# Optimization experiments

Hardware: AMD Instinct MI355X
Metric: run time of the kernel (lower is better)

The kernel has to match this reference:

```python
import jax, jax.numpy as jnp
import numpy as np

B, S, D = 2, 2048, 512
H = 8            # num_attention_heads
CHUNK = 64       # chunk_size
WIN = 128        # retrospective_window / sliding window
NS = 5           # muon_ns_steps
FF = 2048        # intermediate_size
EPS = 1e-6       # RMSNorm eps


def _rms(x, w):
    return x * w * jax.lax.rsqrt(jnp.mean(x * x, axis=-1, keepdims=True) + EPS)


def _dwconv(x, w, b):
    # depthwise conv1d, kernel 3, pad 1. x: [b,s,d], w: [d,3], b: [d]
    xp = jnp.pad(x, ((0, 0), (1, 1), (0, 0)))
    return xp[:, :-2] * w[:, 0] + xp[:, 1:-1] * w[:, 1] + xp[:, 2:] * w[:, 2] + b


def _ns5(G):
    # Muon Newton-Schulz quintic orthogonalization on [b,d,d]
    a, b, c = 3.4445, -4.7750, 2.0315
    X = G / (jnp.linalg.norm(G, axis=(-2, -1), keepdims=True) + 1e-7)
    for _ in range(NS):
        A = X @ jnp.swapaxes(X, -2, -1)
        Bm = b * A + c * (A @ A)
        X = a * X + Bm @ X
    return X


def _swa(x, wq, wk, wv, wo):
    b, s, d = x.shape
    hd = d // H
    q = (x @ wq.T).reshape(b, s, H, hd)
    k = (x @ wk.T).reshape(b, s, H, hd)
    v = (x @ wv.T).reshape(b, s, H, hd)
    scores = jnp.einsum('bqhe,bkhe->bhqk', q, k) / np.float32(np.sqrt(hd))
    i = jnp.arange(s)[:, None]
    j = jnp.arange(s)[None, :]
    mask = (j <= i) & (i - j < WIN)
    scores = jnp.where(mask, scores, -jnp.inf)
    p = jax.nn.softmax(scores, axis=-1)
    o = jnp.einsum('bhqk,bkhe->bqhe', p, v).reshape(b, s, d)
    return o @ wo.T


def setup_inputs() -> dict:
    key = jax.random.key(0)
    ks = jax.random.split(key, 32)
    p = lambda i, shape, s=0.02: jax.random.normal(ks[i], shape, jnp.float32) * s
    inp = {
        'x': jax.random.normal(ks[0], (B, S, D), jnp.float32),
        'mem_state': jnp.zeros((B, D, D), jnp.float32),
        'buf_k': jnp.zeros((B, WIN, D), jnp.float32),
        'buf_v': jnp.zeros((B, WIN, D), jnp.float32),
        'nw_in': jnp.ones((D,), jnp.float32),
        'nw_kq': jnp.ones((D,), jnp.float32),
        'nw_out': jnp.ones((D,), jnp.float32),
        'wk_a': p(1, (D, D)), 'wq_a': p(2, (D, D)), 'wv_a': p(3, (D, D)),
        'wg': p(4, (3 * D, D)), 'wb': p(5, (D, D)),
        'ck_w': p(6, (D, 3), 0.3), 'ck_b': p(7, (D,), 0.02),
        'cq_w': p(8, (D, 3), 0.3), 'cq_b': p(9, (D,), 0.02),
        's1_wq': p(10, (D, D)), 's1_wk': p(11, (D, D)), 's1_wv': p(12, (D, D)), 's1_wo': p(13, (D, D)),
        's2_wq': p(14, (D, D)), 's2_wk': p(15, (D, D)), 's2_wv': p(16, (D, D)), 's2_wo': p(17, (D, D)),
        'n1_w': jnp.ones((D,), jnp.float32), 'n2_w': jnp.ones((D,), jnp.float32),
        'm_w1': p(18, (FF, D)), 'm_w2': p(19, (FF, D)), 'm_w3': p(20, (D, FF)),
    }
    return inp


def _atlas(x, mem_state, buf_k, buf_v, nw_in, nw_kq, nw_out,
           wk_a, wq_a, wv_a, wg, wb, ck_w, ck_b, cq_w, cq_b):
    b, s, d = x.shape
    xn = _rms(x, nw_in)
    v = jax.nn.silu(xn @ wv_a.T)
    k = _rms(jax.nn.silu(_dwconv(xn @ wk_a.T, ck_w, ck_b)), nw_kq)
    q = _rms(jax.nn.silu(_dwconv(xn @ wq_a.T, cq_w, cq_b)), nw_kq)
    gates = jax.nn.silu(xn @ wg.T)
    gamma, eta, alpha = jnp.split(gates, 3, axis=-1)
    bypass = jax.nn.silu(xn @ wb.T)

    n = s // CHUNK
    ch = lambda t: t.reshape(b, n, CHUNK, d).swapaxes(0, 1)  # [n,b,chunk,d]

    def body(carry, inp):
        M, bk, bv = carry
        ck_, cq_, cv_, ce_, ca_ = inp
        ctx_k = jnp.concatenate([bk, ck_], axis=1)
        ctx_v = jnp.concatenate([bv, cv_], axis=1)
        err = ctx_k @ M - ctx_v
        grad = jnp.einsum('bld,ble->bde', ctx_k, err)
        og = _ns5(grad)
        M = M * ca_.mean(axis=1, keepdims=True) - og * ce_.mean(axis=1, keepdims=True)
        return (M, ctx_k[:, -WIN:], ctx_v[:, -WIN:]), cq_ @ M

    (Mf, bkf, bvf), outs = jax.lax.scan(body, (mem_state, buf_k, buf_v),
                                        (ch(k), ch(q), ch(v), ch(eta), ch(alpha)))
    out = outs.swapaxes(0, 1).reshape(b, s, d)
    out = _rms(out, nw_out) * bypass * gamma
    return out, Mf, bkf, bvf


def reference(x, mem_state, buf_k, buf_v, nw_in, nw_kq, nw_out, wk_a, wq_a, wv_a,
              wg, wb, ck_w, ck_b, cq_w, cq_b, s1_wq, s1_wk, s1_wv, s1_wo,
              s2_wq, s2_wk, s2_wv, s2_wo, n1_w, n2_w, m_w1, m_w2, m_w3):
    mem_out, Mf, bkf, bvf = _atlas(x, mem_state, buf_k, buf_v, nw_in, nw_kq, nw_out,
                                   wk_a, wq_a, wv_a, wg, wb, ck_w, ck_b, cq_w, cq_b)
    mem_out = _rms(mem_out, n1_w)
    attn_out = _rms(_swa(x, s1_wq, s1_wk, s1_wv, s1_wo), n2_w)
    fused = mem_out + attn_out
    y = _swa(fused, s2_wq, s2_wk, s2_wv, s2_wo)
    mlp = (jax.nn.silu(y @ m_w1.T) * (y @ m_w2.T)) @ m_w3.T
    out = fused + mlp
    return (out, Mf, bkf, bvf)
```

## Files before the change

### kernel.cpp

```cpp
#include <hip/hip_runtime.h>
#include <hip/hip_bf16.h>

typedef __hip_bfloat16 bf16;
typedef __attribute__((ext_vector_type(8))) short bfrag;
typedef __attribute__((ext_vector_type(8))) unsigned short u16x8;
typedef __attribute__((ext_vector_type(4))) float f32x4;

#define SB 2
#define SS 2048
#define SD 512
#define SH 8
#define SWIN 128
#define SCH 64
#define SNCH 32
#define SFF 2048
#define KPROWS 2176
#define KPBATCH 1114112L
#define BSD 1048576L
#define DD 262144L
#define ERRN 98304L

__device__ __forceinline__ void stf(float* p, float v){ *p = v; }
__device__ __forceinline__ void stf(bf16* p, float v){ *p = __float2bfloat16(v); }

__device__ __forceinline__ unsigned short f2bs(float f){
  union { float f; unsigned int u; } v; v.f = f;
  unsigned int r = v.u + 0x7FFFu + ((v.u >> 16) & 1u);
  return (unsigned short)(r >> 16);
}
__device__ __forceinline__ float bs2f(unsigned short h){
  union { unsigned int u; float f; } v; v.u = ((unsigned int)h) << 16;
  return v.f;
}

__device__ __forceinline__ float block_sum256(float v, float* sbuf){
  #pragma unroll
  for (int o = 32; o > 0; o >>= 1) v += __shfl_xor(v, o);
  int wid = threadIdx.x >> 6;
  if ((threadIdx.x & 63) == 0) sbuf[wid] = v;
  __syncthreads();
  float r = sbuf[0] + sbuf[1] + sbuf[2] + sbuf[3];
  __syncthreads();
  return r;
}

enum { EPI_NONE=0, EPI_SILU=1, EPI_SUB=2, EPI_LINCOMB=3, EPI_MUL=4, EPI_ADD=5, EPI_SILU_MUL=6 };

template<bool TRA, bool TRB, int EPI, bool EPAIR, bool OSPLIT, bool OF32, bool FROB, bool MUPD, int SCL>
__global__ __launch_bounds__(256)
void sgemm32_k(const unsigned short* __restrict__ Ahl, const unsigned short* __restrict__ Bhl,
               float* __restrict__ Cf, unsigned short* __restrict__ Chl,
               const float* __restrict__ Ef, const unsigned short* __restrict__ Ehl,
               float* __restrict__ frobOut,
               const float* __restrict__ partIn, int nPart,
               float a0, float a1, int M, int N, int K,
               long sA, long pA, long sB, long pB,
               long sCf, long sChl, long pC, long sE, long pE,
               int lda, int ldb, int ldc, int lde,
               const float* __restrict__ alphaM, const float* __restrict__ etaM, int chunkIdx)
{
  __shared__ __align__(16) unsigned short As[2][2][32][40];
  __shared__ __align__(16) unsigned short Bs[2][2][32][40];
  __shared__ float fb[4];
  const int bz = blockIdx.z;
  const unsigned short* A = Ahl + (long)bz*sA;
  const unsigned short* B = Bhl + (long)bz*sB;
  const int bm = blockIdx.x*32, bn = blockIdx.y*32;
  const int tid = threadIdx.x;
  const int lane = tid & 63, wid = tid >> 6;
  const int wr = (wid >> 1)*16, wc = (wid & 1)*16;
  const int fm = lane & 15, fk = (lane >> 4)*8;

  int aR=0, aC=0, aPl=0, tK=0, tM0=0, tPl=0;
  if (!TRA) { aR = tid >> 3; int s = tid & 7; aPl = s >> 2; aC = (s & 3) << 3; }
  else      { tK = tid & 31; int q = tid >> 5; tPl = q >> 2; tM0 = (q & 3) << 3; }
  int bR=0, bC=0, bPl=0, uK=0, uN0=0, uPl=0;
  if (TRB)  { bR = tid >> 3; int s = tid & 7; bPl = s >> 2; bC = (s & 3) << 3; }
  else      { uK = tid & 31; int q = tid >> 5; uPl = q >> 2; uN0 = (q & 3) << 3; }

  u16x8 ra, rb;
  auto LA = [&](int k0){
    if (!TRA) ra = *reinterpret_cast<const u16x8*>(A + (long)(bm+aR)*lda + k0 + aC + (aPl ? pA : 0));
    else      ra = *reinterpret_cast<const u16x8*>(A + (long)(k0+tK)*lda + bm + tM0 + (tPl ? pA : 0));
  };
  auto SA = [&](int buf){
    if (!TRA) *reinterpret_cast<u16x8*>(&As[buf][aPl][aR][aC]) = ra;
    else {
      #pragma unroll
      for (int j=0;j<8;j++) As[buf][tPl][tM0+j][tK] = ra[j];
    }
  };
  auto LB = [&](int k0){
    if (TRB)  rb = *reinterpret_cast<const u16x8*>(B + (long)(bn+bR)*ldb + k0 + bC + (bPl ? pB : 0));
    else      rb = *reinterpret_cast<const u16x8*>(B + (long)(k0+uK)*ldb + bn + uN0 + (uPl ? pB : 0));
  };
  auto SBst = [&](int buf){
    if (TRB)  *reinterpret_cast<u16x8*>(&Bs[buf][bPl][bR][bC]) = rb;
    else {
      #pragma unroll
      for (int j=0;j<8;j++) Bs[buf][uPl][uN0+j][uK] = rb[j];
    }
  };

  f32x4 acc = {0.f,0.f,0.f,0.f};
  const int nk = K >> 5;
  LA(0); LB(0);
  int buf = 0;
  for (int i = 0; i < nk; i++) {
    SA(buf); SBst(buf);
    __syncthreads();
    if (i+1 < nk) { LA((i+1)<<5); LB((i+1)<<5); }
    bfrag ah = *reinterpret_cast<const bfrag*>(&As[buf][0][wr+fm][fk]);
    bfrag al = *reinterpret_cast<const bfrag*>(&As[buf][1][wr+fm][fk]);
    bfrag bh = *reinterpret_cast<const bfrag*>(&Bs[buf][0][wc+fm][fk]);
    bfrag bl = *reinterpret_cast<const bfrag*>(&Bs[buf][1][wc+fm][fk]);
    acc = __builtin_amdgcn_mfma_f32_16x16x32_bf16(ah, bh, acc, 0,0,0);
    acc = __builtin_amdgcn_mfma_f32_16x16x32_bf16(ah, bl, acc, 0,0,0);
    acc = __builtin_amdgcn_mfma_f32_16x16x32_bf16(al, bh, acc, 0,0,0);
    buf ^= 1;
  }

  float scl = 1.f;
  if (SCL) {
    float pv = (tid < nPart) ? partIn[(long)bz*nPart + tid] : 0.f;
    __syncthreads();
    float ssum = block_sum256(pv, fb);
    float s = sqrtf(ssum) + 1e-7f;
    scl = (SCL == 1) ? 1.f/(s*s) : 1.f/s;
  }

  const float* alR = MUPD ? (alphaM + ((long)(bz*32 + chunkIdx) << 9)) : nullptr;
  const float* etR = MUPD ? (etaM  + ((long)(bz*32 + chunkIdx) << 9)) : nullptr;

  float fs = 0.f;
  #pragma unroll
  for (int r=0;r<4;r++){
    int row = bm + wr + (lane>>4)*4 + r;
    int col = bn + wc + fm;
    float v = acc[r];
    if (EPI == EPI_SUB || EPI == EPI_LINCOMB) {
      long eidx = (long)bz*sE + (long)row*lde + col;
      float e = EPAIR ? (bs2f(Ehl[eidx]) + bs2f(Ehl[eidx + pE])) : Ef[eidx];
      if (EPI == EPI_SUB) v = v - e;
      else                v = a0*e + a1*v;
    }
    if (SCL) v *= scl;
    if (FROB) fs += v*v;
    if (OF32) Cf[(long)bz*sCf + (long)row*ldc + col] = v;
    if (OSPLIT) {
      long cidx = (long)bz*sChl + (long)row*ldc + col;
      unsigned short h = f2bs(v);
      Chl[cidx]      = h;
      Chl[cidx + pC] = f2bs(v - bs2f(h));
    }
    if (MUPD) {
      long mi = (long)bz*sChl + (long)row*ldc + col;
      float mo = bs2f(Chl[mi]) + bs2f(Chl[mi + pC]);
      float nv = mo*alR[col] - v*etR[col];
      unsigned short h = f2bs(nv);
      Chl[mi]      = h;
      Chl[mi + pC] = f2bs(nv - bs2f(h));
    }
  }
  if (FROB) {
    #pragma unroll
    for (int o = 32; o > 0; o >>= 1) fs += __shfl_xor(fs, o);
    if (lane == 0) fb[wid] = fs;
    __syncthreads();
    if (tid == 0)
      frobOut[(long)bz*(gridDim.x*gridDim.y) + blockIdx.x*gridDim.y + blockIdx.y] =
          fb[0]+fb[1]+fb[2]+fb[3];
  }
}

template<bool TRA, bool TRB, int EPI, bool EPAIR, bool OSPLIT, bool OF32>
__device__ __forceinline__ void gtile(
    const unsigned short* __restrict__ A, long pA, int lda,
    const unsigned short* __restrict__ B, long pB, int ldb,
    float* __restrict__ Cf, unsigned short* __restrict__ Chl, long pC, int ldc,
    const float* __restrict__ Ef, const unsigned short* __restrict__ Ehl, long pE, int lde,
    float a0, float a1,
    int K, int bm, int bn,
    unsigned short (*As)[2][32][40], unsigned short (*Bs)[2][32][40])
{
  const int tid = threadIdx.x;
  const int lane = tid & 63, wid = tid >> 6;
  const int wr = (wid >> 1) * 16, wc = (wid & 1) * 16;
  const int fm = lane & 15, fk = (lane >> 4) * 8;

  int aR=0, aC=0, aPl=0, tK=0, tM0=0, tPl=0;
  if (!TRA) { aR = tid >> 3; int s = tid & 7; aPl = s >> 2; aC = (s & 3) << 3; }
  else      { tK = tid & 31; int q = tid >> 5; tPl = q >> 2; tM0 = (q & 3) << 3; }
  int bR=0, bC=0, bPl=0, uK=0, uN0=0, uPl=0;
  if (TRB)  { bR = tid >> 3; int s = tid & 7; bPl = s >> 2; bC = (s & 3) << 3; }
  else      { uK = tid & 31; int q = tid >> 5; uPl = q >> 2; uN0 = (q & 3) << 3; }

  u16x8 ra, rb;
  auto LA = [&](int k0){
    if (!TRA) ra = *reinterpret_cast<const u16x8*>(A + (long)(bm+aR)*lda + k0 + aC + (aPl ? pA : 0));
    else      ra = *reinterpret_cast<const u16x8*>(A + (long)(k0+tK)*lda + bm + tM0 + (tPl ? pA : 0));
  };
  auto SA = [&](int buf){
    if (!TRA) *reinterpret_cast<u16x8*>(&(*As)[0][0][0] + ((long)buf*2 + aPl)*32*40 + aR*40 + aC) = ra;
    else {
      #pragma unroll
      for (int j=0;j<8;j++) As[buf][tPl][tM0+j][tK] = ra[j];
    }
  };
  auto LB = [&](int k0){
    if (TRB)  rb = *reinterpret_cast<const u16x8*>(B + (long)(bn+bR)*ldb + k0 + bC + (bPl ? pB : 0));
    else      rb = *reinterpret_cast<const u16x8*>(B + (long)(k0+uK)*ldb + bn + uN0 + (uPl ? pB : 0));
  };
  auto SBst = [&](int buf){
    if (TRB)  *reinterpret_cast<u16x8*>(&(*Bs)[0][0][0] + ((long)buf*2 + bPl)*32*40 + bR*40 + bC) = rb;
    else {
      #pragma unroll
      for (int j=0;j<8;j++) Bs[buf][uPl][uN0+j][uK] = rb[j];
    }
  };

  f32x4 acc = {0.f,0.f,0.f,0.f};
  const int nk = K >> 5;
  LA(0); LB(0);
  int buf = 0;
  for (int i = 0; i < nk; i++) {
    SA(buf); SBst(buf);
    __syncthreads();
    if (i+1 < nk) { LA((i+1)<<5); LB((i+1)<<5); }
    bfrag ah = *reinterpret_cast<const bfrag*>(&As[buf][0][wr+fm][fk]);
    bfrag al = *reinterpret_cast<const bfrag*>(&As[buf][1][wr+fm][fk]);
    bfrag bh = *reinterpret_cast<const bfrag*>(&Bs[buf][0][wc+fm][fk]);
    bfrag bl = *reinterpret_cast<const bfrag*>(&Bs[buf][1][wc+fm][fk]);
    acc = __builtin_amdgcn_mfma_f32_16x16x32_bf16(ah, bh, acc, 0,0,0);
    acc = __builtin_amdgcn_mfma_f32_16x16x32_bf16(ah, bl, acc, 0,0,0);
    acc = __builtin_amdgcn_mfma_f32_16x16x32_bf16(al, bh, acc, 0,0,0);
    buf ^= 1;
  }

  #pragma unroll
  for (int r=0;r<4;r++){
    int row = bm + wr + (lane>>4)*4 + r;
    int col = bn + wc + fm;
    float v = acc[r];
    if (EPI == EPI_SUB || EPI == EPI_LINCOMB) {
      float e;
      if (EPAIR){ long ei = (long)row*lde + col; e = bs2f(Ehl[ei]) + bs2f(Ehl[ei + pE]); }
      else      { e = Ef[(long)row*lde + col]; }
      v = (EPI == EPI_SUB) ? (v - e) : (a0*e + a1*v);
    }
    if (OF32) Cf[(long)row*ldc + col] = v;
    if (OSPLIT){
      long ci = (long)row*ldc + col;
      unsigned short h = f2bs(v);
      Chl[ci] = h; Chl[ci + pC] = f2bs(v - bs2f(h));
    }
  }
}

__global__ __launch_bounds__(256)
void out_err_k(const unsigned short* __restrict__ khl,
               const unsigned short* __restrict__ qhl,
               unsigned short* __restrict__ Mhl,
               unsigned short* __restrict__ errhl,
               const float* __restrict__ vp, float* __restrict__ aout,
               int tOut, int tErr)
{
  __shared__ __align__(16) unsigned short As[2][2][32][40];
  __shared__ __align__(16) unsigned short Bs[2][2][32][40];
  int bid = blockIdx.x;
  if (bid < 64) {
    if (tOut < 0) return;
    int b = bid >> 5, r = bid & 31, mt = r >> 4, nt = r & 15;
    long off = (long)tOut*SCH*SD;
    gtile<false,false,EPI_NONE,false,false,true>(
      qhl + (long)b*2*BSD + off, BSD, SD,
      Mhl + (long)b*2*DD, DD, SD,
      aout + (long)b*BSD + off, nullptr, 0, SD,
      nullptr, nullptr, 0, 0,
      0.f,0.f, SD, mt*32, nt*32, As, Bs);
  } else {
    if (tErr >= SNCH) return;
    int ti = bid - 64;
    int b = ti / 96, r = ti % 96, mt = r >> 4, nt = r & 15;
    long off = (long)tErr*SCH*SD;
    gtile<false,false,EPI_SUB,false,true,false>(
      khl + (long)b*2*KPBATCH + off, KPBATCH, SD,
      Mhl + (long)b*2*DD, DD, SD,
      nullptr, errhl + (long)b*2*ERRN, ERRN, SD,
      vp + (long)b*KPBATCH + off, nullptr, 0, SD,
      0.f,0.f, SD, mt*32, nt*32, As, Bs);
  }
}

template<bool TRA, bool TRB, int EPI, typename TO>
__global__ __launch_bounds__(256)
void mgemm_k(const float* __restrict__ Ag, const float* __restrict__ Bg, TO* __restrict__ Cg,
             const float* __restrict__ Eg, float a0, float a1,
             int M, int N, int K,
             long sA, long sB, long sC, long sE,
             int lda, int ldb, int ldc, int lde)
{
  __shared__ __align__(16) unsigned short As[2][64][40];
  __shared__ __align__(16) unsigned short Bs[2][64][40];
  const int bz = blockIdx.z;
  const float* A = Ag + (long)bz*sA;
  const float* Bp = Bg + (long)bz*sB;
  TO* C = Cg + (long)bz*sC;
  const float* E = Eg ? (Eg + (long)bz*sE) : nullptr;
  const int bm = blockIdx.x*64, bn = blockIdx.y*64;
  const int tid = threadIdx.x;
  const int lane = tid & 63, wid = tid >> 6;
  const int wr = (wid >> 1)*32, wc = (wid & 1)*32;
  const int fm = lane & 15, fk = (lane >> 4)*8;

  f32x4 acc[2][2];
  #pragma unroll
  for (int i=0;i<2;i++)
    #pragma unroll
    for (int j=0;j<2;j++) acc[i][j] = (f32x4){0.f,0.f,0.f,0.f};

  for (int k0 = 0; k0 < K; k0 += 32) {
    if (!TRA) {
      int k = tid & 31, m0 = tid >> 5;
      #pragma unroll
      for (int u = 0; u < 8; u++) {
        int m = m0 + u*8;
        float f = A[(long)(bm+m)*lda + k0 + k];
        unsigned short h = f2bs(f);
        As[0][m][k] = h;
        As[1][m][k] = f2bs(f - bs2f(h));
      }
    } else {
      int m = tid & 63, kk0 = tid >> 6;
      #pragma unroll
      for (int u = 0; u < 8; u++) {
        int k = kk0 + u*4;
        float f = A[(long)(k0+k)*lda + bm + m];
        unsigned short h = f2bs(f);
        As[0][m][k] = h;
        As[1][m][k] = f2bs(f - bs2f(h));
      }
    }
    if (TRB) {
      int k = tid & 31, n0 = tid >> 5;
      #pragma unroll
      for (int u = 0; u < 8; u++) {
        int n = n0 + u*8;
        float f = Bp[(long)(bn+n)*ldb + k0 + k];
        unsigned short h = f2bs(f);
        Bs[0][n][k] = h;
        Bs[1][n][k] = f2bs(f - bs2f(h));
      }
    } else {
      int n = tid & 63, kk0 = tid >> 6;
      #pragma unroll
      for (int u = 0; u < 8; u++) {
        int k = kk0 + u*4;
        float f = Bp[(long)(k0+k)*ldb + bn + n];
        unsigned short h = f2bs(f);
        Bs[0][n][k] = h;
        Bs[1][n][k] = f2bs(f - bs2f(h));
      }
    }
    __syncthreads();
    bfrag ah0 = *reinterpret_cast<const bfrag*>(&As[0][wr + fm][fk]);
    bfrag ah1 = *reinterpret_cast<const bfrag*>(&As[0][wr + 16 + fm][fk]);
    bfrag bh0 = *reinterpret_cast<const bfrag*>(&Bs[0][wc + fm][fk]);
    bfrag bh1 = *reinterpret_cast<const bfrag*>(&Bs[0][wc + 16 + fm][fk]);
    bfrag al0 = *reinterpret_cast<const bfrag*>(&As[1][wr + fm][fk]);
    bfrag al1 = *reinterpret_cast<const bfrag*>(&As[1][wr + 16 + fm][fk]);
    bfrag bl0 = *reinterpret_cast<const bfrag*>(&Bs[1][wc + fm][fk]);
    bfrag bl1 = *reinterpret_cast<const bfrag*>(&Bs[1][wc + 16 + fm][fk]);
    acc[0][0] = __builtin_amdgcn_mfma_f32_16x16x32_bf16(ah0, bh0, acc[0][0], 0,0,0);
    acc[0][1] = __builtin_amdgcn_mfma_f32_16x16x32_bf16(ah0, bh1, acc[0][1], 0,0,0);
    acc[1][0] = __builtin_amdgcn_mfma_f32_16x16x32_bf16(ah1, bh0, acc[1][0], 0,0,0);
    acc[1][1] = __builtin_amdgcn_mfma_f32_16x16x32_bf16(ah1, bh1, acc[1][1], 0,0,0);
    acc[0][0] = __builtin_amdgcn_mfma_f32_16x16x32_bf16(ah0, bl0, acc[0][0], 0,0,0);
    acc[0][1] = __builtin_amdgcn_mfma_f32_16x16x32_bf16(ah0, bl1, acc[0][1], 0,0,0);
    acc[1][0] = __builtin_amdgcn_mfma_f32_16x16x32_bf16(ah1, bl0, acc[1][0], 0,0,0);
    acc[1][1] = __builtin_amdgcn_mfma_f32_16x16x32_bf16(ah1, bl1, acc[1][1], 0,0,0);
    acc[0][0] = __builtin_amdgcn_mfma_f32_16x16x32_bf16(al0, bh0, acc[0][0], 0,0,0);
    acc[0][1] = __builtin_amdgcn_mfma_f32_16x16x32_bf16(al0, bh1, acc[0][1], 0,0,0);
    acc[1][0] = __builtin_amdgcn_mfma_f32_16x16x32_bf16(al1, bh0, acc[1][0], 0,0,0);
    acc[1][1] = __builtin_amdgcn_mfma_f32_16x16x32_bf16(al1, bh1, acc[1][1], 0,0,0);
    __syncthreads();
  }

  #pragma unroll
  for (int i=0;i<2;i++) {
// ... 82 lines not shown
  float r = rsqrtf(ss*(1.f/SD) + 1e-6f);
  float t0 = v0*r*nwout[c0] * gb[row*SD+c0];
  float t1 = v1*r*nwout[c1] * gb[row*SD+c1];
  float ss2 = block_sum256(t0*t0 + t1*t1, sbuf);
  float r2 = rsqrtf(ss2*(1.f/SD) + 1e-6f);
  xr[c0] = t0*r2*n1w[c0];
  xr[c1] = t1*r2*n1w[c1];
}

__global__ __launch_bounds__(256) void rms_add_k(const float* __restrict__ o,
    const float* __restrict__ w, float* __restrict__ dst)
{
  __shared__ float sbuf[4];
  long row = blockIdx.x;
  const float* xr = o + row*SD;
  int c0 = threadIdx.x, c1 = threadIdx.x + 256;
  float v0 = xr[c0], v1 = xr[c1];
  float ss = block_sum256(v0*v0 + v1*v1, sbuf);
  float r = rsqrtf(ss*(1.f/SD) + 1e-6f);
  dst[row*SD+c0] += v0*r*w[c0];
  dst[row*SD+c1] += v1*r*w[c1];
}

__global__ __launch_bounds__(256) void attn_swa_k(const float* __restrict__ Q,
    const float* __restrict__ K, const float* __restrict__ V, float* __restrict__ O)
{
  __shared__ float sc[4][SWIN];
  int wid = threadIdx.x >> 6, lane = threadIdx.x & 63;
  int w = blockIdx.x*4 + wid;
  int b = w >> 14;
  int rem = w & 16383;
  int h = rem >> 11;
  int i = rem & (SS-1);
  const float* qp = Q + ((long)b*SS + i)*SD + h*64;
  float qv = qp[lane];
  int j0 = i - (SWIN-1); if (j0 < 0) j0 = 0;
  int cnt = i - j0 + 1;
  const float* Kb = K + (long)b*SS*SD + h*64;
  const float* Vb = V + (long)b*SS*SD + h*64;
  float mx = -1e30f;
  for (int jj = 0; jj < cnt; jj++) {
    float p = qv * Kb[(long)(j0+jj)*SD + lane];
    #pragma unroll
    for (int o2 = 32; o2 > 0; o2 >>= 1) p += __shfl_xor(p, o2);
    p *= 0.125f;
    if (lane == 0) sc[wid][jj] = p;
    mx = fmaxf(mx, p);
  }
  __syncthreads();
  float sum = 0.f, oa = 0.f;
  for (int jj = 0; jj < cnt; jj++) {
    float p = __expf(sc[wid][jj] - mx);
    sum += p;
    oa += p * Vb[(long)(j0+jj)*SD + lane];
  }
  O[((long)b*SS + i)*SD + h*64 + lane] = oa / sum;
}

__global__ __launch_bounds__(256) void copy_f_k(float* __restrict__ dst, long dstride,
    const float* __restrict__ src, long sstride, long nper, int nb)
{
  long total = nper * nb;
  for (long i = (long)blockIdx.x*256 + threadIdx.x; i < total; i += (long)gridDim.x*256) {
    long b = i / nper, r = i - b*nper;
    dst[b*dstride + r] = src[b*sstride + r];
  }
}

__global__ __launch_bounds__(256) void split_k(unsigned short* __restrict__ dst,
    long dBatch, long dPlane, const float* __restrict__ src, long sBatch,
    long nper, int nb)
{
  long total = nper * nb;
  for (long i = (long)blockIdx.x*256 + threadIdx.x; i < total; i += (long)gridDim.x*256) {
    long b = i / nper, r = i - b*nper;
    float f = src[b*sBatch + r];
    unsigned short h = f2bs(f);
    dst[b*dBatch + r]          = h;
    dst[b*dBatch + dPlane + r] = f2bs(f - bs2f(h));
  }
}

__global__ __launch_bounds__(256) void merge_k(float* __restrict__ dst, long dBatch,
    const unsigned short* __restrict__ src, long sBatch, long sPlane, long nper, int nb)
{
  long total = nper * nb;
  for (long i = (long)blockIdx.x*256 + threadIdx.x; i < total; i += (long)gridDim.x*256) {
    long b = i / nper, r = i - b*nper;
    dst[b*dBatch + r] = bs2f(src[b*sBatch + r]) + bs2f(src[b*sBatch + sPlane + r]);
  }
}

extern "C" void kernel_launch(void* const* d_in, const int* in_sizes, int n_in,
                              void* d_out, int out_size, void* d_ws, size_t ws_size,
                              hipStream_t stream)
{
  (void)in_sizes; (void)n_in; (void)out_size; (void)ws_size;
  const float* x      = (const float*)d_in[0];
  const float* mem0   = (const float*)d_in[1];
  const float* buf_k  = (const float*)d_in[2];
  const float* buf_v  = (const float*)d_in[3];
  const float* nw_in  = (const float*)d_in[4];
  const float* nw_kq  = (const float*)d_in[5];
  const float* nw_out = (const float*)d_in[6];
  const float* wk_a   = (const float*)d_in[7];
  const float* wq_a   = (const float*)d_in[8];
  const float* wv_a   = (const float*)d_in[9];
  const float* wg     = (const float*)d_in[10];
  const float* wb     = (const float*)d_in[11];
  const float* ck_w   = (const float*)d_in[12];
  const float* ck_b   = (const float*)d_in[13];
  const float* cq_w   = (const float*)d_in[14];
  const float* cq_b   = (const float*)d_in[15];
  const float* s1_wq  = (const float*)d_in[16];
  const float* s1_wk  = (const float*)d_in[17];
  const float* s1_wv  = (const float*)d_in[18];
  const float* s1_wo  = (const float*)d_in[19];
  const float* s2_wq  = (const float*)d_in[20];
  const float* s2_wk  = (const float*)d_in[21];
  const float* s2_wv  = (const float*)d_in[22];
  const float* s2_wo  = (const float*)d_in[23];
  const float* n1_w   = (const float*)d_in[24];
  const float* n2_w   = (const float*)d_in[25];
  const float* m_w1   = (const float*)d_in[26];
  const float* m_w2   = (const float*)d_in[27];
  const float* m_w3   = (const float*)d_in[28];
  float* ob = (float*)d_out;

  float* p = (float*)d_ws;
  float* kp   = p; p += SB*KPBATCH;
  float* vp   = p; p += SB*KPBATCH;
  float* qbuf = p; p += SB*BSD;
  float* gb   = p; p += SB*BSD;
  float* sc1  = p; p += SB*BSD;
  float* sc2  = p; p += SB*BSD;
  float* Mb   = p; p += SB*DD;
  float* etaM = p; p += (long)SB*SNCH*SD;
  float* alphaM = p; p += (long)SB*SNCH*SD;
  float* partials = p; p += 512;
  unsigned short* us = (unsigned short*)p;
  unsigned short* khl = us; us += SB*2*KPBATCH;
  unsigned short* qhl = us; us += SB*2*BSD;
  unsigned short* Mhl = us; us += SB*2*DD;
  unsigned short* Xhl = us; us += SB*2*DD;
  unsigned short* Yhl = us; us += SB*2*DD;
  unsigned short* Ahl = us; us += SB*2*DD;
  unsigned short* Thl = us; us += SB*2*DD;
  unsigned short* errhl = us; us += SB*2*ERRN;
  float* nsbuf = (float*)khl;
  float* aout = sc2;
  float* hbuf = kp;

  dim3 blk(256);

  rmsnorm_in_k<<<SB*SS, blk, 0, stream>>>(x, nw_in, sc1);

  mgemm_k<false,true,EPI_SILU,float><<<dim3(32,8,2),blk,0,stream>>>(
      sc1, wv_a, vp + (long)SWIN*SD, nullptr, 0.f,0.f, SS, SD, SD,
      BSD, 0, KPBATCH, 0, SD, SD, SD, 0);

  mgemm_k<false,true,EPI_NONE,float><<<dim3(64,8,1),blk,0,stream>>>(
      sc1, wk_a, sc2, nullptr, 0.f,0.f, SB*SS, SD, SD, 0,0,0,0, SD,SD,SD,0);
  conv_silu_rms_k<<<dim3(SS,SB),blk,0,stream>>>(sc2, ck_w, ck_b, nw_kq, kp, KPBATCH, SWIN);

  mgemm_k<false,true,EPI_NONE,float><<<dim3(64,8,1),blk,0,stream>>>(
      sc1, wq_a, sc2, nullptr, 0.f,0.f, SB*SS, SD, SD, 0,0,0,0, SD,SD,SD,0);
  conv_silu_rms_k<<<dim3(SS,SB),blk,0,stream>>>(sc2, cq_w, cq_b, nw_kq, qbuf, BSD, 0);

  mgemm_k<false,true,EPI_SILU,float><<<dim3(64,8,1),blk,0,stream>>>(
      sc1, wg, gb, nullptr, 0.f,0.f, SB*SS, SD, SD, 0,0,0,0, SD,SD,SD,0);
  mgemm_k<false,true,EPI_SILU_MUL,float><<<dim3(64,8,1),blk,0,stream>>>(
      sc1, wb, gb, gb, 0.f,0.f, SB*SS, SD, SD, 0,0,0,0, SD,SD,SD,SD);

  mgemm_k<false,true,EPI_SILU,float><<<dim3(64,8,1),blk,0,stream>>>(
      sc1, wg + (long)SD*SD, nsbuf, nullptr, 0.f,0.f, SB*SS, SD, SD, 0,0,0,0, SD,SD,SD,0);
  chunk_means1_k<<<SB*SNCH, blk, 0, stream>>>(nsbuf, etaM);
  mgemm_k<false,true,EPI_SILU,float><<<dim3(64,8,1),blk,0,stream>>>(
      sc1, wg + 2L*SD*SD, nsbuf, nullptr, 0.f,0.f, SB*SS, SD, SD, 0,0,0,0, SD,SD,SD,0);
  chunk_means1_k<<<SB*SNCH, blk, 0, stream>>>(nsbuf, alphaM);

  copy_f_k<<<256,blk,0,stream>>>(kp, KPBATCH, buf_k, (long)SWIN*SD, (long)SWIN*SD, SB);
  copy_f_k<<<256,blk,0,stream>>>(vp, KPBATCH, buf_v, (long)SWIN*SD, (long)SWIN*SD, SB);
  copy_f_k<<<256,blk,0,stream>>>(Mb, DD, mem0, DD, DD, SB);

  split_k<<<512,blk,0,stream>>>(khl, 2*KPBATCH, KPBATCH, kp, KPBATCH, KPBATCH, SB);
  split_k<<<512,blk,0,stream>>>(qhl, 2*BSD, BSD, qbuf, BSD, BSD, SB);
  split_k<<<256,blk,0,stream>>>(Mhl, 2*DD, DD, Mb, DD, DD, SB);

  out_err_k<<<256,blk,0,stream>>>(khl, qhl, Mhl, errhl, vp, aout, -1, 0);

  for (int t = 0; t < SNCH; ++t) {
    const long off = (long)t*SCH*SD;
    sgemm32_k<true,false,EPI_NONE,false,true,false,true,false,0><<<dim3(16,16,2),blk,0,stream>>>(
        khl + off, errhl, nullptr, Xhl, nullptr, nullptr, partials, nullptr, 0,
        0.f,0.f, 512, 512, 192,
        2*KPBATCH, KPBATCH, 2*ERRN, ERRN,
        0, 2*DD, DD, 0, 0,
        512,512,512,0, nullptr, nullptr, 0);
    sgemm32_k<false,true,EPI_NONE,false,true,false,false,false,1><<<dim3(16,16,2),blk,0,stream>>>(
        Xhl, Xhl, nullptr, Ahl, nullptr, nullptr, nullptr, partials, 256,
        0.f,0.f, 512,512,512, 2*DD,DD, 2*DD,DD, 0, 2*DD,DD, 0,0, 512,512,512,0,
        nullptr, nullptr, 0);
    sgemm32_k<false,true,EPI_LINCOMB,true,true,false,false,false,0><<<dim3(16,16,2),blk,0,stream>>>(
        Ahl, Ahl, nullptr, Thl, nullptr, Ahl, nullptr, nullptr, 0,
        -4.7750f, 2.0315f, 512,512,512, 2*DD,DD, 2*DD,DD, 0, 2*DD,DD, 2*DD,DD,
        512,512,512,512, nullptr, nullptr, 0);
    sgemm32_k<false,false,EPI_LINCOMB,true,true,false,false,false,2><<<dim3(16,16,2),blk,0,stream>>>(
        Thl, Xhl, nullptr, Yhl, nullptr, Xhl, nullptr, partials, 256,
        3.4445f, 1.0f, 512,512,512, 2*DD,DD, 2*DD,DD, 0, 2*DD,DD, 2*DD,DD,
        512,512,512,512, nullptr, nullptr, 0);
    unsigned short* Xc = Yhl; unsigned short* Xn = Xhl;
    for (int it = 0; it < 3; ++it) {
      sgemm32_k<false,true,EPI_NONE,false,true,false,false,false,0><<<dim3(16,16,2),blk,0,stream>>>(
          Xc, Xc, nullptr, Ahl, nullptr, nullptr, nullptr, nullptr, 0,
          0.f,0.f, 512,512,512, 2*DD,DD, 2*DD,DD, 0, 2*DD,DD, 0,0, 512,512,512,0,
          nullptr, nullptr, 0);
      sgemm32_k<false,true,EPI_LINCOMB,true,true,false,false,false,0><<<dim3(16,16,2),blk,0,stream>>>(
          Ahl, Ahl, nullptr, Thl, nullptr, Ahl, nullptr, nullptr, 0,
          -4.7750f, 2.0315f, 512,512,512, 2*DD,DD, 2*DD,DD, 0, 2*DD,DD, 2*DD,DD,
          512,512,512,512, nullptr, nullptr, 0);
      sgemm32_k<false,false,EPI_LINCOMB,true,true,false,false,false,0><<<dim3(16,16,2),blk,0,stream>>>(
          Thl, Xc, nullptr, Xn, nullptr, Xc, nullptr, nullptr, 0,
          3.4445f, 1.0f, 512,512,512, 2*DD,DD, 2*DD,DD, 0, 2*DD,DD, 2*DD,DD,
          512,512,512,512, nullptr, nullptr, 0);
      unsigned short* tmp = Xc; Xc = Xn; Xn = tmp;
    }
    sgemm32_k<false,true,EPI_NONE,false,true,false,false,false,0><<<dim3(16,16,2),blk,0,stream>>>(
        Xc, Xc, nullptr, Ahl, nullptr, nullptr, nullptr, nullptr, 0,
        0.f,0.f, 512,512,512, 2*DD,DD, 2*DD,DD, 0, 2*DD,DD, 0,0, 512,512,512,0,
        nullptr, nullptr, 0);
    sgemm32_k<false,true,EPI_LINCOMB,true,true,false,false,false,0><<<dim3(16,16,2),blk,0,stream>>>(
        Ahl, Ahl, nullptr, Thl, nullptr, Ahl, nullptr, nullptr, 0,
        -4.7750f, 2.0315f, 512,512,512, 2*DD,DD, 2*DD,DD, 0, 2*DD,DD, 2*DD,DD,
        512,512,512,512, nullptr, nullptr, 0);
    sgemm32_k<false,false,EPI_LINCOMB,true,false,false,false,true,0><<<dim3(16,16,2),blk,0,stream>>>(
        Thl, Xc, nullptr, Mhl, nullptr, Xc, nullptr, nullptr, 0,
        3.4445f, 1.0f, 512,512,512, 2*DD,DD, 2*DD,DD, 0, 2*DD, DD, 2*DD,DD,
        512,512,512,512, alphaM, etaM, t);
    out_err_k<<<256,blk,0,stream>>>(khl, qhl, Mhl, errhl, vp, aout, t, t+1);
  }

  atlas_final_norm_k<<<SB*SS,blk,0,stream>>>(sc2, gb, nw_out, n1_w);

  merge_k<<<256,blk,0,stream>>>(ob + (long)SB*SS*SD, DD, Mhl, 2*DD, DD, DD, SB);
  copy_f_k<<<256,blk,0,stream>>>(ob + (long)SB*SS*SD + SB*DD, (long)SWIN*SD,
      kp + (long)SS*SD, KPBATCH, (long)SWIN*SD, SB);
  copy_f_k<<<256,blk,0,stream>>>(ob + (long)SB*SS*SD + SB*DD + (long)SB*SWIN*SD, (long)SWIN*SD,
      vp + (long)SS*SD, KPBATCH, (long)SWIN*SD, SB);

  mgemm_k<false,true,EPI_NONE,float><<<dim3(64,8,1),blk,0,stream>>>(
      x, s1_wq, sc1, nullptr,0.f,0.f, SB*SS, SD, SD, 0,0,0,0, SD,SD,SD,0);
  mgemm_k<false,true,EPI_NONE,float><<<dim3(64,8,1),blk,0,stream>>>(
      x, s1_wk, gb, nullptr,0.f,0.f, SB*SS, SD, SD, 0,0,0,0, SD,SD,SD,0);
  mgemm_k<false,true,EPI_NONE,float><<<dim3(64,8,1),blk,0,stream>>>(
      x, s1_wv, qbuf, nullptr,0.f,0.f, SB*SS, SD, SD, 0,0,0,0, SD,SD,SD,0);
  attn_swa_k<<<SB*SH*SS/4, blk, 0, stream>>>(sc1, gb, qbuf, kp);
  mgemm_k<false,true,EPI_NONE,float><<<dim3(64,8,1),blk,0,stream>>>(
      kp, s1_wo, vp, nullptr,0.f,0.f, SB*SS, SD, SD, 0,0,0,0, SD,SD,SD,0);
  rms_add_k<<<SB*SS,blk,0,stream>>>(vp, n2_w, sc2);

  mgemm_k<false,true,EPI_NONE,float><<<dim3(64,8,1),blk,0,stream>>>(
      sc2, s2_wq, sc1, nullptr,0.f,0.f, SB*SS, SD, SD, 0,0,0,0, SD,SD,SD,0);
  mgemm_k<false,true,EPI_NONE,float><<<dim3(64,8,1),blk,0,stream>>>(
      sc2, s2_wk, gb, nullptr,0.f,0.f, SB*SS, SD, SD, 0,0,0,0, SD,SD,SD,0);
  mgemm_k<false,true,EPI_NONE,float><<<dim3(64,8,1),blk,0,stream>>>(
      sc2, s2_wv, qbuf, nullptr,0.f,0.f, SB*SS, SD, SD, 0,0,0,0, SD,SD,SD,0);
  attn_swa_k<<<SB*SH*SS/4, blk, 0, stream>>>(sc1, gb, qbuf, kp);
  mgemm_k<false,true,EPI_NONE,float><<<dim3(64,8,1),blk,0,stream>>>(
      kp, s2_wo, sc1, nullptr,0.f,0.f, SB*SS, SD, SD, 0,0,0,0, SD,SD,SD,0);

  mgemm_k<false,true,EPI_SILU,float><<<dim3(64,32,1),blk,0,stream>>>(
      sc1, m_w1, hbuf, nullptr,0.f,0.f, SB*SS, SFF, SD, 0,0,0,0, SD,SD,SFF,0);
  mgemm_k<false,true,EPI_MUL,float><<<dim3(64,32,1),blk,0,stream>>>(
      sc1, m_w2, hbuf, hbuf, 0.f,0.f, SB*SS, SFF, SD, 0,0,0,0, SD,SD,SFF,SFF);
  mgemm_k<false,true,EPI_ADD,float><<<dim3(64,8,1),blk,0,stream>>>(
      hbuf, m_w3, ob, sc2, 0.f,0.f, SB*SS, SD, SFF, 0,0,0,0, SFF,SFF,SD,SD);
}
```

Before: 6.220 ms.

## Split K across two warp groups in sequential-scan Newton-Schulz GEMMs

Replaces the 256-thread 32x32-tile split-bf16 GEMM used in the per-chunk Muon scan with a 512-thread variant in which two groups of four waves each handle half of the K dimension. The partial accumulators are reduced through shared memory before the epilogue. The scan launches only 512 small blocks per GEMM, and this aims to raise per-block parallelism and latency hiding on these latency-bound launches. In exchange it adds an extra barrier per K step, a shared-memory reduction, and more LDS per block. The gtile helper also gains a trailing sync per K step.

Measured after the change: 5.737 ms. -7.8%, faster.

```diff
diff --git a/kernel.cpp b/kernel.cpp
--- a/kernel.cpp
+++ b/kernel.cpp
@@ -47,29 +47,170 @@
 enum { EPI_NONE=0, EPI_SILU=1, EPI_SUB=2, EPI_LINCOMB=3, EPI_MUL=4, EPI_ADD=5, EPI_SILU_MUL=6 };
 
 template<bool TRA, bool TRB, int EPI, bool EPAIR, bool OSPLIT, bool OF32, bool FROB, bool MUPD, int SCL>
-__global__ __launch_bounds__(256)
-void sgemm32_k(const unsigned short* __restrict__ Ahl, const unsigned short* __restrict__ Bhl,
-               float* __restrict__ Cf, unsigned short* __restrict__ Chl,
-               const float* __restrict__ Ef, const unsigned short* __restrict__ Ehl,
-               float* __restrict__ frobOut,
-               const float* __restrict__ partIn, int nPart,
-               float a0, float a1, int M, int N, int K,
-               long sA, long pA, long sB, long pB,
-               long sCf, long sChl, long pC, long sE, long pE,
-               int lda, int ldb, int ldc, int lde,
-               const float* __restrict__ alphaM, const float* __restrict__ etaM, int chunkIdx)
-{
-  __shared__ __align__(16) unsigned short As[2][2][32][40];
-  __shared__ __align__(16) unsigned short Bs[2][2][32][40];
-  __shared__ float fb[4];
+__global__ __launch_bounds__(512)
+void sgemm32s_k(const unsigned short* __restrict__ Ahl, const unsigned short* __restrict__ Bhl,
+                float* __restrict__ Cf, unsigned short* __restrict__ Chl,
+                const float* __restrict__ Ef, const unsigned short* __restrict__ Ehl,
+                float* __restrict__ frobOut,
+                const float* __restrict__ partIn, int nPart,
+                float a0, float a1, int M, int N, int K,
+                long sA, long pA, long sB, long pB,
+                long sCf, long sChl, long pC, long sE, long pE,
+                int lda, int ldb, int ldc, int lde,
+                const float* __restrict__ alphaM, const float* __restrict__ etaM, int chunkIdx)
+{
+  __shared__ __align__(16) unsigned short As[2][2][2][32][40];
+  __shared__ __align__(16) unsigned short Bs[2][2][2][32][40];
+  __shared__ float accx[4][64][4];
+  __shared__ float sb8[8];
   const int bz = blockIdx.z;
   const unsigned short* A = Ahl + (long)bz*sA;
   const unsigned short* B = Bhl + (long)bz*sB;
   const int bm = blockIdx.x*32, bn = blockIdx.y*32;
   const int tid = threadIdx.x;
+  const int lane = tid & 63, w = tid >> 6;
+  const int q = w & 3, kh = w >> 2;
+  const int wr = (q >> 1)*16, wc = (q & 1)*16;
+  const int fm = lane & 15, fk = (lane >> 4)*8;
+  const int htid = tid & 255;
+  const int kbase = kh * (K >> 1);
+  const int nk2 = K >> 6;
+
+  int aR=0, aC=0, aPl=0, tK=0, tM0=0, tPl=0;
+  if (!TRA) { aR = htid >> 3; int s = htid & 7; aPl = s >> 2; aC = (s & 3) << 3; }
+  else      { tK = htid & 31; int qq = htid >> 5; tPl = qq >> 2; tM0 = (qq & 3) << 3; }
+  int bR=0, bC=0, bPl=0, uK=0, uN0=0, uPl=0;
+  if (TRB)  { bR = htid >> 3; int s = htid & 7; bPl = s >> 2; bC = (s & 3) << 3; }
+  else      { uK = htid & 31; int qq = htid >> 5; uPl = qq >> 2; uN0 = (qq & 3) << 3; }
+
+  u16x8 ra, rb;
+  auto LA = [&](int k0){
+    int kk = kbase + k0;
+    if (!TRA) ra = *reinterpret_cast<const u16x8*>(A + (long)(bm+aR)*lda + kk + aC + (aPl ? pA : 0));
+    else      ra = *reinterpret_cast<const u16x8*>(A + (long)(kk+tK)*lda + bm + tM0 + (tPl ? pA : 0));
+  };
+  auto SA = [&](int buf){
+    if (!TRA) *reinterpret_cast<u16x8*>(&As[kh][buf][aPl][aR][aC]) = ra;
+    else {
+      #pragma unroll
+      for (int j=0;j<8;j++) As[kh][buf][tPl][tM0+j][tK] = ra[j];
+    }
+  };
+  auto LB = [&](int k0){
+    int kk = kbase + k0;
+    if (TRB)  rb = *reinterpret_cast<const u16x8*>(B + (long)(bn+bR)*ldb + kk + bC + (bPl ? pB : 0));
+    else      rb = *reinterpret_cast<const u16x8*>(B + (long)(kk+uK)*ldb + bn + uN0 + (uPl ? pB : 0));
+  };
+  auto SBst = [&](int buf){
+    if (TRB)  *reinterpret_cast<u16x8*>(&Bs[kh][buf][bPl][bR][bC]) = rb;
+    else {
+      #pragma unroll
+      for (int j=0;j<8;j++) Bs[kh][buf][uPl][uN0+j][uK] = rb[j];
+    }
+  };
+
+  f32x4 acc = {0.f,0.f,0.f,0.f};
+  LA(0); LB(0);
+  int buf = 0;
+  for (int i = 0; i < nk2; i++) {
+    SA(buf); SBst(buf);
+    __syncthreads();
+    if (i+1 < nk2) { LA((i+1)<<5); LB((i+1)<<5); }
+    bfrag ah = *reinterpret_cast<const bfrag*>(&As[kh][buf][0][wr+fm][fk]);
+    bfrag al = *reinterpret_cast<const bfrag*>(&As[kh][buf][1][wr+fm][fk]);
+    bfrag bh = *reinterpret_cast<const bfrag*>(&Bs[kh][buf][0][wc+fm][fk]);
+    bfrag bl = *reinterpret_cast<const bfrag*>(&Bs[kh][buf][1][wc+fm][fk]);
+    acc = __builtin_amdgcn_mfma_f32_16x16x32_bf16(ah, bh, acc, 0,0,0);
+    acc = __builtin_amdgcn_mfma_f32_16x16x32_bf16(ah, bl, acc, 0,0,0);
+    acc = __builtin_amdgcn_mfma_f32_16x16x32_bf16(al, bh, acc, 0,0,0);
+    buf ^= 1;
+    __syncthreads();
+  }
+
+  if (kh == 1) {
+    #pragma unroll
+    for (int r=0;r<4;r++) accx[q][lane][r] = acc[r];
+  }
+  __syncthreads();
+  float accv[4];
+  if (kh == 0) {
+    #pragma unroll
+    for (int r=0;r<4;r++) accv[r] = acc[r] + accx[q][lane][r];
+  }
+
+  float scl = 1.f;
+  if (SCL) {
+    float pv = (tid < nPart) ? partIn[(long)bz*nPart + tid] : 0.f;
+    #pragma unroll
+    for (int o = 32; o > 0; o >>= 1) pv += __shfl_xor(pv, o);
+    if (lane == 0) sb8[w] = pv;
+    __syncthreads();
+    float ssum = sb8[0]+sb8[1]+sb8[2]+sb8[3]+sb8[4]+sb8[5]+sb8[6]+sb8[7];
+    float s = sqrtf(ssum) + 1e-7f;
+    scl = (SCL == 1) ? 1.f/(s*s) : 1.f/s;
+    __syncthreads();
+  }
+
+  const float* alR = MUPD ? (alphaM + ((long)(bz*32 + chunkIdx) << 9)) : nullptr;
+  const float* etR = MUPD ? (etaM  + ((long)(bz*32 + chunkIdx) << 9)) : nullptr;
+
+  float fs = 0.f;
+  if (kh == 0) {
+    #pragma unroll
+    for (int r=0;r<4;r++){
+      int row = bm + wr + (lane>>4)*4 + r;
+      int col = bn + wc + fm;
+      float v = accv[r];
+      if (EPI == EPI_SUB || EPI == EPI_LINCOMB) {
+        long eidx = (long)bz*sE + (long)row*lde + col;
+        float e = EPAIR ? (bs2f(Ehl[eidx]) + bs2f(Ehl[eidx + pE])) : Ef[eidx];
+        if (EPI == EPI_SUB) v = v - e;
+        else                v = a0*e + a1*v;
+      }
+      if (SCL) v *= scl;
+      if (FROB) fs += v*v;
+      if (OF32) Cf[(long)bz*sCf + (long)row*ldc + col] = v;
+      if (OSPLIT) {
+        long cidx = (long)bz*sChl + (long)row*ldc + col;
+        unsigned short h = f2bs(v);
+        Chl[cidx]      = h;
+        Chl[cidx + pC] = f2bs(v - bs2f(h));
+      }
+      if (MUPD) {
+        long mi = (long)bz*sChl + (long)row*ldc + col;
+        float mo = bs2f(Chl[mi]) + bs2f(Chl[mi + pC]);
+        float nv = mo*alR[col] - v*etR[col];
+        unsigned short h = f2bs(nv);
+        Chl[mi]      = h;
+        Chl[mi + pC] = f2bs(nv - bs2f(h));
+      }
+    }
+  }
+  if (FROB) {
+    #pragma unroll
+    for (int o = 32; o > 0; o >>= 1) fs += __shfl_xor(fs, o);
+    if (lane == 0) sb8[w] = fs;
+    __syncthreads();
+    if (tid == 0)
+      frobOut[(long)bz*(gridDim.x*gridDim.y) + blockIdx.x*gridDim.y + blockIdx.y] =
+          sb8[0]+sb8[1]+sb8[2]+sb8[3]+sb8[4]+sb8[5]+sb8[6]+sb8[7];
+  }
+}
+
+template<bool TRA, bool TRB, int EPI, bool EPAIR, bool OSPLIT, bool OF32>
+__device__ __forceinline__ void gtile(
+    const unsigned short* __restrict__ A, long pA, int lda,
+    const unsigned short* __restrict__ B, long pB, int ldb,
+    float* __restrict__ Cf, unsigned short* __restrict__ Chl, long pC, int ldc,
+    const float* __restrict__ Ef, const unsigned short* __restrict__ Ehl, long pE, int lde,
+    float a0, float a1,
+    int K, int bm, int bn,
+    unsigned short (*As)[2][32][40], unsigned short (*Bs)[2][32][40])
+{
+  const int tid = threadIdx.x;
   const int lane = tid & 63, wid = tid >> 6;
-  const int wr = (wid >> 1)*16, wc = (wid & 1)*16;
-  const int fm = lane & 15, fk = (lane >> 4)*8;
+  const int wr = (wid >> 1) * 16, wc = (wid & 1) * 16;
+  const int fm = lane & 15, fk = (lane >> 4) * 8;
 
   int aR=0, aC=0, aPl=0, tK=0, tM0=0, tPl=0;
   if (!TRA) { aR = tid >> 3; int s = tid & 7; aPl = s >> 2; aC = (s & 3) << 3; }
@@ -84,7 +225,7 @@
     else      ra = *reinterpret_cast<const u16x8*>(A + (long)(k0+tK)*lda + bm + tM0 + (tPl ? pA : 0));
   };
   auto SA = [&](int buf){
-    if (!TRA) *reinterpret_cast<u16x8*>(&As[buf][aPl][aR][aC]) = ra;
+    if (!TRA) *reinterpret_cast<u16x8*>(&(*As)[0][0][0] + ((long)buf*2 + aPl)*32*40 + aR*40 + aC) = ra;
     else {
       #pragma unroll
       for (int j=0;j<8;j++) As[buf][tPl][tM0+j][tK] = ra[j];
@@ -95,7 +236,7 @@
     else      rb = *reinterpret_cast<const u16x8*>(B + (long)(k0+uK)*ldb + bn + uN0 + (uPl ? pB : 0));
   };
   auto SBst = [&](int buf){
-    if (TRB)  *reinterpret_cast<u16x8*>(&Bs[buf][bPl][bR][bC]) = rb;
+    if (TRB)  *reinterpret_cast<u16x8*>(&(*Bs)[0][0][0] + ((long)buf*2 + bPl)*32*40 + bR*40 + bC) = rb;
     else {
       #pragma unroll
       for (int j=0;j<8;j++) Bs[buf][uPl][uN0+j][uK] = rb[j];
@@ -118,123 +259,7 @@
     acc = __builtin_amdgcn_mfma_f32_16x16x32_bf16(ah, bl, acc, 0,0,0);
     acc = __builtin_amdgcn_mfma_f32_16x16x32_bf16(al, bh, acc, 0,0,0);
     buf ^= 1;
-  }
-
-  float scl = 1.f;
-  if (SCL) {
-    float pv = (tid < nPart) ? partIn[(long)bz*nPart + tid] : 0.f;
-    __syncthreads();
-    float ssum = block_sum256(pv, fb);
-    float s = sqrtf(ssum) + 1e-7f;
-    scl = (SCL == 1) ? 1.f/(s*s) : 1.f/s;
-  }
-
-  const float* alR = MUPD ? (alphaM + ((long)(bz*32 + chunkIdx) << 9)) : nullptr;
-  const float* etR = MUPD ? (etaM  + ((long)(bz*32 + chunkIdx) << 9)) : nullptr;
-
-  float fs = 0.f;
-  #pragma unroll
-  for (int r=0;r<4;r++){
-    int row = bm + wr + (lane>>4)*4 + r;
-    int col = bn + wc + fm;
-    float v = acc[r];
-    if (EPI == EPI_SUB || EPI == EPI_LINCOMB) {
-      long eidx = (long)bz*sE + (long)row*lde + col;
-      float e = EPAIR ? (bs2f(Ehl[eidx]) + bs2f(Ehl[eidx + pE])) : Ef[eidx];
-      if (EPI == EPI_SUB) v = v - e;
-      else                v = a0*e + a1*v;
-    }
-    if (SCL) v *= scl;
-    if (FROB) fs += v*v;
-    if (OF32) Cf[(long)bz*sCf + (long)row*ldc + col] = v;
-    if (OSPLIT) {
-      long cidx = (long)bz*sChl + (long)row*ldc + col;
-      unsigned short h = f2bs(v);
-      Chl[cidx]      = h;
-      Chl[cidx + pC] = f2bs(v - bs2f(h));
-    }
-    if (MUPD) {
-      long mi = (long)bz*sChl + (long)row*ldc + col;
-      float mo = bs2f(Chl[mi]) + bs2f(Chl[mi + pC]);
-      float nv = mo*alR[col] - v*etR[col];
-      unsigned short h = f2bs(nv);
-      Chl[mi]      = h;
-      Chl[mi + pC] = f2bs(nv - bs2f(h));
-    }
-  }
-  if (FROB) {
-    #pragma unroll
-    for (int o = 32; o > 0; o >>= 1) fs += __shfl_xor(fs, o);
-    if (lane == 0) fb[wid] = fs;
-    __syncthreads();
-    if (tid == 0)
-      frobOut[(long)bz*(gridDim.x*gridDim.y) + blockIdx.x*gridDim.y + blockIdx.y] =
-          fb[0]+fb[1]+fb[2]+fb[3];
-  }
-}
-
-template<bool TRA, bool TRB, int EPI, bool EPAIR, bool OSPLIT, bool OF32>
-__device__ __forceinline__ void gtile(
-    const unsigned short* __restrict__ A, long pA, int lda,
-    const unsigned short* __restrict__ B, long pB, int ldb,
-    float* __restrict__ Cf, unsigned short* __restrict__ Chl, long pC, int ldc,
-    const float* __restrict__ Ef, const unsigned short* __restrict__ Ehl, long pE, int lde,
-    float a0, float a1,
-    int K, int bm, int bn,
-    unsigned short (*As)[2][32][40], unsigned short (*Bs)[2][32][40])
-{
-  const int tid = threadIdx.x;
-  const int lane = tid & 63, wid = tid >> 6;
-  const int wr = (wid >> 1) * 16, wc = (wid & 1) * 16;
-  const int fm = lane & 15, fk = (lane >> 4) * 8;
-
-  int aR=0, aC=0, aPl=0, tK=0, tM0=0, tPl=0;
-  if (!TRA) { aR = tid >> 3; int s = tid & 7; aPl = s >> 2; aC = (s & 3) << 3; }
-  else      { tK = tid & 31; int q = tid >> 5; tPl = q >> 2; tM0 = (q & 3) << 3; }
-  int bR=0, bC=0, bPl=0, uK=0, uN0=0, uPl=0;
-  if (TRB)  { bR = tid >> 3; int s = tid & 7; bPl = s >> 2; bC = (s & 3) << 3; }
-  else      { uK = tid & 31; int q = tid >> 5; uPl = q >> 2; uN0 = (q & 3) << 3; }
-
-  u16x8 ra, rb;
-  auto LA = [&](int k0){
-    if (!TRA) ra = *reinterpret_cast<const u16x8*>(A + (long)(bm+aR)*lda + k0 + aC + (aPl ? pA : 0));
-    else      ra = *reinterpret_cast<const u16x8*>(A + (long)(k0+tK)*lda + bm + tM0 + (tPl ? pA : 0));
-  };
-  auto SA = [&](int buf){
-    if (!TRA) *reinterpret_cast<u16x8*>(&(*As)[0][0][0] + ((long)buf*2 + aPl)*32*40 + aR*40 + aC) = ra;
-    else {
-      #pragma unroll
-      for (int j=0;j<8;j++) As[buf][tPl][tM0+j][tK] = ra[j];
-    }
-  };
-  auto LB = [&](int k0){
-    if (TRB)  rb = *reinterpret_cast<const u16x8*>(B + (long)(bn+bR)*ldb + k0 + bC + (bPl ? pB : 0));
-    else      rb = *reinterpret_cast<const u16x8*>(B + (long)(k0+uK)*ldb + bn + uN0 + (uPl ? pB : 0));
-  };
-  auto SBst = [&](int buf){
-    if (TRB)  *reinterpret_cast<u16x8*>(&(*Bs)[0][0][0] + ((long)buf*2 + bPl)*32*40 + bR*40 + bC) = rb;
-    else {
-      #pragma unroll
-      for (int j=0;j<8;j++) Bs[buf][uPl][uN0+j][uK] = rb[j];
-    }
-  };
-
-  f32x4 acc = {0.f,0.f,0.f,0.f};
-  const int nk = K >> 5;
-  LA(0); LB(0);
-  int buf = 0;
-  for (int i = 0; i < nk; i++) {
-    SA(buf); SBst(buf);
-    __syncthreads();
-    if (i+1 < nk) { LA((i+1)<<5); LB((i+1)<<5); }
-    bfrag ah = *reinterpret_cast<const bfrag*>(&As[buf][0][wr+fm][fk]);
-    bfrag al = *reinterpret_cast<const bfrag*>(&As[buf][1][wr+fm][fk]);
-    bfrag bh = *reinterpret_cast<const bfrag*>(&Bs[buf][0][wc+fm][fk]);
-    bfrag bl = *reinterpret_cast<const bfrag*>(&Bs[buf][1][wc+fm][fk]);
-    acc = __builtin_amdgcn_mfma_f32_16x16x32_bf16(ah, bh, acc, 0,0,0);
-    acc = __builtin_amdgcn_mfma_f32_16x16x32_bf16(ah, bl, acc, 0,0,0);
-    acc = __builtin_amdgcn_mfma_f32_16x16x32_bf16(al, bh, acc, 0,0,0);
-    buf ^= 1;
+    __syncthreads();
   }
 
   #pragma unroll
@@ -623,6 +648,7 @@
   float* hbuf = kp;
 
   dim3 blk(256);
+  dim3 blk512(512);
 
   rmsnorm_in_k<<<SB*SS, blk, 0, stream>>>(x, nw_in, sc1);
 
@@ -662,49 +688,49 @@
 
   for (int t = 0; t < SNCH; ++t) {
     const long off = (long)t*SCH*SD;
-    sgemm32_k<true,false,EPI_NONE,false,true,false,true,false,0><<<dim3(16,16,2),blk,0,stream>>>(
+    sgemm32s_k<true,false,EPI_NONE,false,true,false,true,false,0><<<dim3(16,16,2),blk512,0,stream>>>(
         khl + off, errhl, nullptr, Xhl, nullptr, nullptr, partials, nullptr, 0,
         0.f,0.f, 512, 512, 192,
         2*KPBATCH, KPBATCH, 2*ERRN, ERRN,
         0, 2*DD, DD, 0, 0,
         512,512,512,0, nullptr, nullptr, 0);
-    sgemm32_k<false,true,EPI_NONE,false,true,false,false,false,1><<<dim3(16,16,2),blk,0,stream>>>(
+    sgemm32s_k<false,true,EPI_NONE,false,true,false,false,false,1><<<dim3(16,16,2),blk512,0,stream>>>(
         Xhl, Xhl, nullptr, Ahl, nullptr, nullptr, nullptr, partials, 256,
         0.f,0.f, 512,512,512, 2*DD,DD, 2*DD,DD, 0, 2*DD,DD, 0,0, 512,512,512,0,
         nullptr, nullptr, 0);
-    sgemm32_k<false,true,EPI_LINCOMB,true,true,false,false,false,0><<<dim3(16,16,2),blk,0,stream>>>(
+    sgemm32s_k<false,true,EPI_LINCOMB,true,true,false,false,false,0><<<dim3(16,16,2),blk512,0,stream>>>(
         Ahl, Ahl, nullptr, Thl, nullptr, Ahl, nullptr, nullptr, 0,
         -4.7750f, 2.0315f, 512,512,512, 2*DD,DD, 2*DD,DD, 0, 2*DD,DD, 2*DD,DD,
         512,512,512,512, nullptr, nullptr, 0);
-    sgemm32_k<false,false,EPI_LINCOMB,true,true,false,false,false,2><<<dim3(16,16,2),blk,0,stream>>>(
+    sgemm32s_k<false,false,EPI_LINCOMB,true,true,false,false,false,2><<<dim3(16,16,2),blk512,0,stream>>>(
         Thl, Xhl, nullptr, Yhl, nullptr, Xhl, nullptr, partials, 256,
         3.4445f, 1.0f, 512,512,512, 2*DD,DD, 2*DD,DD, 0, 2*DD,DD, 2*DD,DD,
         512,512,512,512, nullptr, nullptr, 0);
     unsigned short* Xc = Yhl; unsigned short* Xn = Xhl;
     for (int it = 0; it < 3; ++it) {
-      sgemm32_k<false,true,EPI_NONE,false,true,false,false,false,0><<<dim3(16,16,2),blk,0,stream>>>(
+      sgemm32s_k<false,true,EPI_NONE,false,true,false,false,false,0><<<dim3(16,16,2),blk512,0,stream>>>(
           Xc, Xc, nullptr, Ahl, nullptr, nullptr, nullptr, nullptr, 0,
           0.f,0.f, 512,512,512, 2*DD,DD, 2*DD,DD, 0, 2*DD,DD, 0,0, 512,512,512,0,
           nullptr, nullptr, 0);
-      sgemm32_k<false,true,EPI_LINCOMB,true,true,false,false,false,0><<<dim3(16,16,2),blk,0,stream>>>(
+      sgemm32s_k<false,true,EPI_LINCOMB,true,true,false,false,false,0><<<dim3(16,16,2),blk512,0,stream>>>(
           Ahl, Ahl, nullptr, Thl, nullptr, Ahl, nullptr, nullptr, 0,
           -4.7750f, 2.0315f, 512,512,512, 2*DD,DD, 2*DD,DD, 0, 2*DD,DD, 2*DD,DD,
           512,512,512,512, nullptr, nullptr, 0);
-      sgemm32_k<false,false,EPI_LINCOMB,true,true,false,false,false,0><<<dim3(16,16,2),blk,0,stream>>>(
+      sgemm32s_k<false,false,EPI_LINCOMB,true,true,false,false,false,0><<<dim3(16,16,2),blk512,0,stream>>>(
           Thl, Xc, nullptr, Xn, nullptr, Xc, nullptr, nullptr, 0,
           3.4445f, 1.0f, 512,512,512, 2*DD,DD, 2*DD,DD, 0, 2*DD,DD, 2*DD,DD,
           512,512,512,512, nullptr, nullptr, 0);
       unsigned short* tmp = Xc; Xc = Xn; Xn = tmp;
     }
-    sgemm32_k<false,true,EPI_NONE,false,true,false,false,false,0><<<dim3(16,16,2),blk,0,stream>>>(
+    sgemm32s_k<false,true,EPI_NONE,false,true,false,false,false,0><<<dim3(16,16,2),blk512,0,stream>>>(
         Xc, Xc, nullptr, Ahl, nullptr, nullptr, nullptr, nullptr, 0,
         0.f,0.f, 512,512,512, 2*DD,DD, 2*DD,DD, 0, 2*DD,DD, 0,0, 512,512,512,0,
         nullptr, nullptr, 0);
-    sgemm32_k<false,true,EPI_LINCOMB,true,true,false,false,false,0><<<dim3(16,16,2),blk,0,stream>>>(
+    sgemm32s_k<false,true,EPI_LINCOMB,true,true,false,false,false,0><<<dim3(16,16,2),blk512,0,stream>>>(
         Ahl, Ahl, nullptr, Thl, nullptr, Ahl, nullptr, nullptr, 0,
         -4.7750f, 2.0315f, 512,512,512, 2*DD,DD, 2*DD,DD, 0, 2*DD,DD, 2*DD,DD,
         512,512,512,512, nullptr, nullptr, 0);
-    sgemm32_k<false,false,EPI_LINCOMB,true,false,false,false,true,0><<<dim3(16,16,2),blk,0,stream>>>(
+    sgemm32s_k<false,false,EPI_LINCOMB,true,false,false,false,true,0><<<dim3(16,16,2),blk512,0,stream>>>(
         Thl, Xc, nullptr, Mhl, nullptr, Xc, nullptr, nullptr, 0,
         3.4445f, 1.0f, 512,512,512, 2*DD,DD, 2*DD,DD, 0, 2*DD, DD, 2*DD,DD,
         512,512,512,512, alphaM, etaM, t);
```
